# Kernel tuning notes

Measured on AMD Instinct MI355X. Metric: run time of the kernel, lower is better.

## Reference

```python
import jax, jax.numpy as jnp
import numpy as np

# ---- module hyperparameters (match init_kwargs) ----
SPATIAL = (32, 64)          # token grid, N = 32*64 = 2048
D_MODEL = 1024
N_HEADS = 16
HEAD_DIM = D_MODEL // N_HEADS  # 64
THETA = 10000.0
XPOS_SCALE_BASE = SPATIAL[0] * 2  # 64


def _rope_tables():
    """ND rotary (xpos) tables, lucidrains-style.
    Each spatial axis gets head_dim//ndim rotary channels; frequencies are
    interleave-repeated (r=2) to pair with rotate_half. Returns cos, sin,
    xpos scale, each [N, HEAD_DIM] float32."""
    nd = len(SPATIAL)
    dpa = HEAD_DIM // nd  # dims per axis (32)
    freqs_axes, scale_axes = [], []
    for size in SPATIAL:
        inv_freq = 1.0 / (THETA ** (np.arange(0, dpa, 2, dtype=np.float64) / dpa))
        t = np.arange(size, dtype=np.float64)
        f = np.repeat(t[:, None] * inv_freq[None, :], 2, axis=-1)        # [size, dpa]
        sbase = (np.arange(0, dpa, 2, dtype=np.float64) + 0.4 * dpa) / (1.4 * dpa)
        power = (t - size // 2) / XPOS_SCALE_BASE
        sc = np.repeat(sbase[None, :] ** power[:, None], 2, axis=-1)     # [size, dpa]
        freqs_axes.append(f)
        scale_axes.append(sc)
    # broadcast each axis table over the full grid, concat along channel dim
    def grid_concat(tabs):
        parts = []
        for i, tab in enumerate(tabs):
            shp = [1] * nd + [dpa]
            shp[i] = SPATIAL[i]
            parts.append(np.broadcast_to(tab.reshape(shp), tuple(SPATIAL) + (dpa,)))
        return np.concatenate(parts, axis=-1).reshape(-1, HEAD_DIM)  # [N, HEAD_DIM]
    freqs = grid_concat(freqs_axes)
    xscale = grid_concat(scale_axes)
    return (jnp.asarray(np.cos(freqs), jnp.float32),
            jnp.asarray(np.sin(freqs), jnp.float32),
            jnp.asarray(xscale, jnp.float32))


def _rotate_half(x):
    # pairwise rotation: (x1, x2) -> (-x2, x1), interleaved layout
    x = x.reshape(*x.shape[:-1], -1, 2)
    x1, x2 = x[..., 0], x[..., 1]
    return jnp.stack((-x2, x1), axis=-1).reshape(*x.shape[:-2], -1)


def setup_inputs() -> dict:
    key = jax.random.key(0)
    ks = jax.random.split(key, 3)
    B, N = 2, SPATIAL[0] * SPATIAL[1]
    x = jax.random.normal(ks[0], (B, N, D_MODEL), dtype=jnp.float32)
    w_qkv = jax.random.normal(ks[1], (D_MODEL, 3 * D_MODEL), dtype=jnp.float32) * 0.02
    b_qkv = jnp.zeros((3 * D_MODEL,), jnp.float32)
    w_proj = jax.random.normal(ks[2], (D_MODEL, D_MODEL), dtype=jnp.float32) * 0.02
    b_proj = jnp.zeros((D_MODEL,), jnp.float32)
    return {"x": x, "w_qkv": w_qkv, "b_qkv": b_qkv, "w_proj": w_proj, "b_proj": b_proj}


def reference(x, w_qkv, b_qkv, w_proj, b_proj):
    B, N, C = x.shape
    scale = HEAD_DIM ** -0.5
    qkv = (x @ w_qkv + b_qkv).reshape(B, N, 3, N_HEADS, HEAD_DIM)
    qkv = qkv.transpose(2, 0, 3, 1, 4)  # [3, B, H, N, D]
    q, k, v = qkv[0], qkv[1], qkv[2]
    cos, sin, xs = _rope_tables()       # [N, D], broadcast over B,H
    q = (q * cos + _rotate_half(q) * sin) * xs
    k = (k * cos + _rotate_half(k) * sin) / xs
    attn = jax.nn.softmax(jnp.einsum('bhnd,bhmd->bhnm', q, k) * scale, axis=-1)
    out = jnp.einsum('bhnm,bhmd->bhnd', attn, v)
    out = out.transpose(0, 2, 1, 3).reshape(B, N, C)
    return out @ w_proj + b_proj
```

## Files before the change

kernel.cpp:

```cpp
#include <hip/hip_runtime.h>
#include <math.h>

typedef __attribute__((ext_vector_type(8))) _Float16 f16x8;
typedef __attribute__((ext_vector_type(4))) _Float16 f16x4;
typedef __attribute__((ext_vector_type(4))) float f32x4;

#define MFMAH(a, b, c) __builtin_amdgcn_mfma_f32_16x16x32_f16((a), (b), (c), 0, 0, 0)

#define QSCALE 0.18033688011112042f
#define SOFF 4.328085122666891f


__global__ void cast_f16_kernel(const float* __restrict__ in, _Float16* __restrict__ out, int n) {
    int i = blockIdx.x * 256 + threadIdx.x;
    if (i >= n) return;
    out[i] = (_Float16)in[i];
}

__global__ void transpose_cast_f16_kernel(const float* __restrict__ in,
                                          _Float16* __restrict__ out, int C) {
    int i = blockIdx.x * 256 + threadIdx.x;
    if (i >= (C << 10)) return;
    int c = i >> 10;
    int r = i & 1023;
    out[i] = (_Float16)in[(size_t)r * C + c];
}

__global__ void rope_tables_kernel(float* __restrict__ ct, float* __restrict__ st,
                                   float* __restrict__ xt) {
    int i = blockIdx.x * 256 + threadIdx.x;
    if (i >= 2048 * 64) return;
    int n = i >> 6, d = i & 63;
    int gi = n >> 6, gj = n & 63;
    int axis = d >> 5;
    int p = (d & 31) >> 1;
    float t = axis ? (float)gj : (float)gi;
    float half = axis ? 32.0f : 16.0f;
    float inv_freq = powf(10000.0f, -(float)p * (1.0f / 16.0f));
    float fr = t * inv_freq;
    float sbase = (2.0f * p + 12.8f) / 44.8f;
    float xs = powf(sbase, (t - half) * (1.0f / 64.0f));
    ct[i] = cosf(fr);
    st[i] = sinf(fr);
    xt[i] = xs;
}

#define LDK 40

__global__ __launch_bounds__(256) void gemm_qkv_kernel(
    const _Float16* __restrict__ A_g, const _Float16* __restrict__ B_g,
    const float* __restrict__ bias, const float* __restrict__ ctab,
    const float* __restrict__ stab, const float* __restrict__ xtab,
    _Float16* __restrict__ qb, _Float16* __restrict__ kb, _Float16* __restrict__ vt) {
    __shared__ __align__(16) _Float16 Asm[128 * LDK];
    __shared__ __align__(16) _Float16 Bsm[128 * LDK];

    const int tid = threadIdx.x;
    const int lane = tid & 63, wave = tid >> 6;
    const int quad = lane >> 4, l16 = lane & 15;
    const int wm = wave >> 1, wn = wave & 1;
    const int m0 = blockIdx.x * 128, n0 = blockIdx.y * 128;

    f32x4 zero = {0.f, 0.f, 0.f, 0.f};
    f32x4 acc[4][4];
#pragma unroll
    for (int i = 0; i < 4; ++i)
#pragma unroll
        for (int j = 0; j < 4; ++j) acc[i][j] = zero;

    const int r0 = tid >> 2, o0 = (tid & 3) << 3;
    const int r1 = (tid + 256) >> 2, o1 = ((tid + 256) & 3) << 3;

    for (int k0 = 0; k0 < 1024; k0 += 32) {
        const size_t ab = (size_t)m0 * 1024 + k0;
        const size_t bb = (size_t)n0 * 1024 + k0;
        *(f16x8*)&Asm[r0 * LDK + o0] = *(const f16x8*)&A_g[ab + (size_t)r0 * 1024 + o0];
        *(f16x8*)&Asm[r1 * LDK + o1] = *(const f16x8*)&A_g[ab + (size_t)r1 * 1024 + o1];
        *(f16x8*)&Bsm[r0 * LDK + o0] = *(const f16x8*)&B_g[bb + (size_t)r0 * 1024 + o0];
        *(f16x8*)&Bsm[r1 * LDK + o1] = *(const f16x8*)&B_g[bb + (size_t)r1 * 1024 + o1];
        __syncthreads();

        f16x8 af[4], bf[4];
#pragma unroll
        for (int i = 0; i < 4; ++i) {
            af[i] = *(const f16x8*)&Asm[(wm * 64 + i * 16 + l16) * LDK + quad * 8];
            bf[i] = *(const f16x8*)&Bsm[(wn * 64 + i * 16 + l16) * LDK + quad * 8];
        }
#pragma unroll
        for (int i = 0; i < 4; ++i)
#pragma unroll
            for (int j = 0; j < 4; ++j) acc[i][j] = MFMAH(af[i], bf[j], acc[i][j]);
        __syncthreads();
    }

    float bj[4];
#pragma unroll
    for (int j = 0; j < 4; ++j) bj[j] = bias[n0 + wn * 64 + j * 16 + l16];

    if (n0 < 2048) {
#pragma unroll
        for (int i = 0; i < 4; ++i) {
#pragma unroll
            for (int r = 0; r < 4; ++r) {
                const int row = m0 + wm * 64 + i * 16 + quad * 4 + r;
                const int b = row >> 11, nrow = row & 2047;
#pragma unroll
                for (int j = 0; j < 4; ++j) {
                    const int col = n0 + wn * 64 + j * 16 + l16;
                    float v = acc[i][j][r] + bj[j];
                    float partner = __shfl_xor(v, 1);
                    const int hh = (col >> 6) & 15;
                    const int d = col & 63;
                    const size_t o = ((size_t)(b * 16 + hh) * 2048 + nrow) * 64 + d;
                    float rh = (d & 1) ? partner : -partner;
                    const int ti = nrow * 64 + d;
                    float rv = v * ctab[ti] + rh * stab[ti];
                    float xs = xtab[ti];
                    if (col < 1024)
                        qb[o] = (_Float16)(rv * xs * QSCALE);
                    else
                        kb[o] = (_Float16)(rv / xs);
                }
            }
        }
    } else {
#pragma unroll
        for (int i = 0; i < 4; ++i) {
            const int row = m0 + wm * 64 + i * 16 + quad * 4;
            const int b = row >> 11, nrow = row & 2047;
#pragma unroll
            for (int j = 0; j < 4; ++j) {
                const int col = n0 + wn * 64 + j * 16 + l16;
                const int hh = (col >> 6) & 15;
                const int d = col & 63;
                f16x4 pv4;
#pragma unroll
                for (int r = 0; r < 4; ++r) pv4[r] = (_Float16)(acc[i][j][r] + bj[j]);
                *(f16x4*)&vt[((size_t)(b * 16 + hh) * 64 + d) * 2048 + nrow] = pv4;
            }
        }
    }
}

__global__ __launch_bounds__(256) void gemm_proj_kernel(
    const _Float16* __restrict__ A_g, const _Float16* __restrict__ B_g,
    const float* __restrict__ bias, float* __restrict__ out) {
    __shared__ __align__(16) _Float16 Asm[128 * LDK];
    __shared__ __align__(16) _Float16 Bsm[128 * LDK];

    const int tid = threadIdx.x;
    const int lane = tid & 63, wave = tid >> 6;
    const int quad = lane >> 4, l16 = lane & 15;
    const int wm = wave >> 1, wn = wave & 1;
    const int m0 = blockIdx.x * 128, n0 = blockIdx.y * 128;

    f32x4 zero = {0.f, 0.f, 0.f, 0.f};
    f32x4 acc[4][4];
#pragma unroll
    for (int i = 0; i < 4; ++i)
#pragma unroll
        for (int j = 0; j < 4; ++j) acc[i][j] = zero;

    const int r0 = tid >> 2, o0 = (tid & 3) << 3;
    const int r1 = (tid + 256) >> 2, o1 = ((tid + 256) & 3) << 3;

    for (int k0 = 0; k0 < 1024; k0 += 32) {
        const size_t ab = (size_t)m0 * 1024 + k0;
        const size_t bb = (size_t)n0 * 1024 + k0;
        *(f16x8*)&Asm[r0 * LDK + o0] = *(const f16x8*)&A_g[ab + (size_t)r0 * 1024 + o0];
        *(f16x8*)&Asm[r1 * LDK + o1] = *(const f16x8*)&A_g[ab + (size_t)r1 * 1024 + o1];
        *(f16x8*)&Bsm[r0 * LDK + o0] = *(const f16x8*)&B_g[bb + (size_t)r0 * 1024 + o0];
        *(f16x8*)&Bsm[r1 * LDK + o1] = *(const f16x8*)&B_g[bb + (size_t)r1 * 1024 + o1];
        __syncthreads();

        f16x8 af[4], bf[4];
#pragma unroll
        for (int i = 0; i < 4; ++i) {
            af[i] = *(const f16x8*)&Asm[(wm * 64 + i * 16 + l16) * LDK + quad * 8];
            bf[i] = *(const f16x8*)&Bsm[(wn * 64 + i * 16 + l16) * LDK + quad * 8];
        }
#pragma unroll
        for (int i = 0; i < 4; ++i)
#pragma unroll
            for (int j = 0; j < 4; ++j) acc[i][j] = MFMAH(af[i], bf[j], acc[i][j]);
        __syncthreads();
    }

    float bj[4];
#pragma unroll
    for (int j = 0; j < 4; ++j) bj[j] = bias[n0 + wn * 64 + j * 16 + l16];
#pragma unroll
    for (int i = 0; i < 4; ++i)
#pragma unroll
        for (int r = 0; r < 4; ++r) {
            const int row = m0 + wm * 64 + i * 16 + quad * 4 + r;
#pragma unroll
            for (int j = 0; j < 4; ++j) {
                const int col = n0 + wn * 64 + j * 16 + l16;
                out[(size_t)row * 1024 + col] = acc[i][j][r] + bj[j];
            }
        }
}

#define KLD 72
#define PLD 72

__global__ __launch_bounds__(256) void attn_kernel(
    const _Float16* __restrict__ qb, const _Float16* __restrict__ kb,
    const _Float16* __restrict__ vt, _Float16* __restrict__ ao) {
    __shared__ __align__(16) _Float16 Ksm[64 * KLD];
    __shared__ __align__(16) _Float16 Vsm[64 * KLD];
    __shared__ __align__(16) _Float16 Psm[4 * 32 * PLD];

    const int tid = threadIdx.x;
    const int lane = tid & 63, wave = tid >> 6;
    const int quad = lane >> 4, l16 = lane & 15;
    const int qt = blockIdx.x & 15, bh = blockIdx.x >> 4;
    const size_t base = (size_t)bh * 2048 * 64;
    const int qrow0 = qt * 128 + wave * 32;

    f16x8 qf[2][2];
#pragma unroll
    for (int rg = 0; rg < 2; ++rg) {
        qf[rg][0] = *(const f16x8*)&qb[base + (size_t)(qrow0 + rg * 16 + l16) * 64 + quad * 8];
        qf[rg][1] = *(const f16x8*)&qb[base + (size_t)(qrow0 + rg * 16 + l16) * 64 + 32 + quad * 8];
    }

    f32x4 zero = {0.f, 0.f, 0.f, 0.f};
    f32x4 moff = {-SOFF, -SOFF, -SOFF, -SOFF};
    f32x4 o[2][4];
    float lsum[2] = {0.f, 0.f};
#pragma unroll
    for (int rg = 0; rg < 2; ++rg)
#pragma unroll
        for (int dc = 0; dc < 4; ++dc) o[rg][dc] = zero;

    const int kr0 = tid >> 3, ko0 = (tid & 7) << 3;
    const int kr1 = (tid + 256) >> 3, ko1 = ((tid + 256) & 7) << 3;
    f16x8 pk[2], pv[2];

    pk[0] = *(const f16x8*)&kb[base + (size_t)kr0 * 64 + ko0];
    pk[1] = *(const f16x8*)&kb[base + (size_t)kr1 * 64 + ko1];
    pv[0] = *(const f16x8*)&vt[((size_t)bh * 64 + kr0) * 2048 + ko0];
    pv[1] = *(const f16x8*)&vt[((size_t)bh * 64 + kr1) * 2048 + ko1];

    _Float16* Pw = &Psm[wave * 32 * PLD];

    for (int it = 0; it < 32; ++it) {
        __syncthreads();
        *(f16x8*)&Ksm[kr0 * KLD + ko0] = pk[0];
        *(f16x8*)&Ksm[kr1 * KLD + ko1] = pk[1];
        *(f16x8*)&Vsm[kr0 * KLD + ko0] = pv[0];
        *(f16x8*)&Vsm[kr1 * KLD + ko1] = pv[1];
        __syncthreads();

        if (it + 1 < 32) {
            const int kt = (it + 1) * 64;
            pk[0] = *(const f16x8*)&kb[base + (size_t)(kt + kr0) * 64 + ko0];
            pk[1] = *(const f16x8*)&kb[base + (size_t)(kt + kr1) * 64 + ko1];
            pv[0] = *(const f16x8*)&vt[((size_t)bh * 64 + kr0) * 2048 + kt + ko0];
            pv[1] = *(const f16x8*)&vt[((size_t)bh * 64 + kr1) * 2048 + kt + ko1];
        }

        f32x4 s[2][4];
#pragma unroll
        for (int kg = 0; kg < 4; ++kg) {
            f16x8 kf0 = *(const f16x8*)&Ksm[(kg * 16 + l16) * KLD + quad * 8];
            f16x8 kf1 = *(const f16x8*)&Ksm[(kg * 16 + l16) * KLD + 32 + quad * 8];
            s[0][kg] = MFMAH(kf0, qf[0][0], moff);
            s[0][kg] = MFMAH(kf1, qf[0][1], s[0][kg]);
            s[1][kg] = MFMAH(kf0, qf[1][0], moff);
            s[1][kg] = MFMAH(kf1, qf[1][1], s[1][kg]);
        }

#pragma unroll
        for (int rg = 0; rg < 2; ++rg)
#pragma unroll
            for (int kg = 0; kg < 4; ++kg) {
                float p0 = __builtin_amdgcn_exp2f(s[rg][kg][0]);
                float p1 = __builtin_amdgcn_exp2f(s[rg][kg][1]);
                float p2 = __builtin_amdgcn_exp2f(s[rg][kg][2]);
                float p3 = __builtin_amdgcn_exp2f(s[rg][kg][3]);
                lsum[rg] += (p0 + p1) + (p2 + p3);
                f16x4 ph = {(_Float16)p0, (_Float16)p1, (_Float16)p2, (_Float16)p3};
                *(f16x4*)&Pw[(rg * 16 + l16) * PLD + kg * 16 + quad * 4] = ph;
            }

        f16x8 pf[2][2];
#pragma unroll
        for (int rg = 0; rg < 2; ++rg) {
            pf[rg][0] = *(const f16x8*)&Pw[(rg * 16 + l16) * PLD + quad * 8];
            pf[rg][1] = *(const f16x8*)&Pw[(rg * 16 + l16) * PLD + 32 + quad * 8];
        }
#pragma unroll
        for (int dc = 0; dc < 4; ++dc) {
            f16x8 vf0 = *(const f16x8*)&Vsm[(dc * 16 + l16) * KLD + quad * 8];
            f16x8 vf1 = *(const f16x8*)&Vsm[(dc * 16 + l16) * KLD + 32 + quad * 8];
#pragma unroll
            for (int rg = 0; rg < 2; ++rg) {
                o[rg][dc] = MFMAH(pf[rg][0], vf0, o[rg][dc]);
                o[rg][dc] = MFMAH(pf[rg][1], vf1, o[rg][dc]);
            }
        }
    }

    float linv[2][4];
#pragma unroll
    for (int rg = 0; rg < 2; ++rg) {
        float v = lsum[rg];
        v += __shfl_xor(v, 16);
        v += __shfl_xor(v, 32);
        v = 1.0f / v;
#pragma unroll
        for (int r = 0; r < 4; ++r) linv[rg][r] = __shfl(v, quad * 4 + r);
    }

    const int b = bh >> 4, hh = bh & 15;
#pragma unroll
    for (int rg = 0; rg < 2; ++rg)
#pragma unroll
        for (int dc = 0; dc < 4; ++dc)
#pragma unroll
            for (int r = 0; r < 4; ++r) {
                float v = o[rg][dc][r] * linv[rg][r];
                const int qrow = qrow0 + rg * 16 + quad * 4 + r;
                const size_t oi = ((size_t)(b * 2048 + qrow)) * 1024 + hh * 64 + dc * 16 + l16;
                ao[oi] = (_Float16)v;
            }
}

extern "C" void kernel_launch(void* const* d_in, const int* in_sizes, int n_in,
                              void* d_out, int out_size, void* d_ws, size_t ws_size,
                              hipStream_t stream) {
    const float* x = (const float*)d_in[0];
    const float* w_qkv = (const float*)d_in[1];
    const float* b_qkv = (const float*)d_in[2];
    const float* w_proj = (const float*)d_in[3];
    const float* b_proj = (const float*)d_in[4];
    float* out = (float*)d_out;

    char* ws = (char*)d_ws;
    size_t off = 0;
    auto take = [&](size_t bytes) { char* p = ws + off; off += bytes; return p; };
    _Float16* xbuf   = (_Float16*)take(8388608);
    _Float16* wqkvT  = (_Float16*)take(6291456);
    _Float16* wprojT = (_Float16*)take(2097152);
    _Float16* qbuf   = (_Float16*)take(8388608);
    _Float16* kbuf   = (_Float16*)take(8388608);
    _Float16* vtbuf  = (_Float16*)take(8388608);
    float* ctab      = (float*)take(524288);
    float* stab      = (float*)take(524288);
    float* xtab      = (float*)take(524288);
    _Float16* ao = xbuf;

    cast_f16_kernel<<<16384, 256, 0, stream>>>(x, xbuf, 4194304);
    transpose_cast_f16_kernel<<<12288, 256, 0, stream>>>(w_qkv, wqkvT, 3072);
    transpose_cast_f16_kernel<<<4096, 256, 0, stream>>>(w_proj, wprojT, 1024);
    rope_tables_kernel<<<512, 256, 0, stream>>>(ctab, stab, xtab);
    gemm_qkv_kernel<<<dim3(32, 24), 256, 0, stream>>>(xbuf, wqkvT, b_qkv,
                                                      ctab, stab, xtab, qbuf, kbuf, vtbuf);
    attn_kernel<<<512, 256, 0, stream>>>(qbuf, kbuf, vtbuf, ao);
    gemm_proj_kernel<<<dim3(32, 8), 256, 0, stream>>>(ao, wprojT, b_proj, out);
}
```

Measured before the change: 241.5 us.

## Double-buffer LDS in GEMMs and attention, fuse prep kernels, retile projection

Merges the four preprocessing kernels (casts, weight transposes, RoPE tables) into one launch. The QKV GEMM, projection GEMM and attention kernel now double-buffer shared memory, so the global loads for the next tile overlap MFMA work on the current one. The projection GEMM drops to 128x64 tiles to launch more blocks, and the attention block index is reordered so consecutive blocks cover different heads. This costs more LDS per block, which may lower occupancy.

After: 217.3 us. 1.11x faster.

```diff
diff --git a/kernel.cpp b/kernel.cpp
--- a/kernel.cpp
+++ b/kernel.cpp
@@ -10,39 +10,39 @@
 #define QSCALE 0.18033688011112042f
 #define SOFF 4.328085122666891f
 
-
-__global__ void cast_f16_kernel(const float* __restrict__ in, _Float16* __restrict__ out, int n) {
-    int i = blockIdx.x * 256 + threadIdx.x;
-    if (i >= n) return;
-    out[i] = (_Float16)in[i];
-}
-
-__global__ void transpose_cast_f16_kernel(const float* __restrict__ in,
-                                          _Float16* __restrict__ out, int C) {
-    int i = blockIdx.x * 256 + threadIdx.x;
-    if (i >= (C << 10)) return;
-    int c = i >> 10;
-    int r = i & 1023;
-    out[i] = (_Float16)in[(size_t)r * C + c];
-}
-
-__global__ void rope_tables_kernel(float* __restrict__ ct, float* __restrict__ st,
-                                   float* __restrict__ xt) {
-    int i = blockIdx.x * 256 + threadIdx.x;
-    if (i >= 2048 * 64) return;
-    int n = i >> 6, d = i & 63;
-    int gi = n >> 6, gj = n & 63;
-    int axis = d >> 5;
-    int p = (d & 31) >> 1;
-    float t = axis ? (float)gj : (float)gi;
-    float half = axis ? 32.0f : 16.0f;
-    float inv_freq = powf(10000.0f, -(float)p * (1.0f / 16.0f));
-    float fr = t * inv_freq;
-    float sbase = (2.0f * p + 12.8f) / 44.8f;
-    float xs = powf(sbase, (t - half) * (1.0f / 64.0f));
-    ct[i] = cosf(fr);
-    st[i] = sinf(fr);
-    xt[i] = xs;
+__global__ void prep_kernel(const float* __restrict__ x, const float* __restrict__ w_qkv,
+                            const float* __restrict__ w_proj, _Float16* __restrict__ xb,
+                            _Float16* __restrict__ wq, _Float16* __restrict__ wp,
+                            float* __restrict__ ct, float* __restrict__ st,
+                            float* __restrict__ xt) {
+    const int b = blockIdx.x, tid = threadIdx.x;
+    if (b < 16384) {
+        int i = b * 256 + tid;
+        xb[i] = (_Float16)x[i];
+    } else if (b < 28672) {
+        int i = (b - 16384) * 256 + tid;
+        int c = i >> 10, r = i & 1023;
+        wq[i] = (_Float16)w_qkv[(size_t)r * 3072 + c];
+    } else if (b < 32768) {
+        int i = (b - 28672) * 256 + tid;
+        int c = i >> 10, r = i & 1023;
+        wp[i] = (_Float16)w_proj[(size_t)r * 1024 + c];
+    } else {
+        int i = (b - 32768) * 256 + tid;
+        int n = i >> 6, d = i & 63;
+        int gi = n >> 6, gj = n & 63;
+        int axis = d >> 5;
+        int p = (d & 31) >> 1;
+        float t = axis ? (float)gj : (float)gi;
+        float half = axis ? 32.0f : 16.0f;
+        float inv_freq = powf(10000.0f, -(float)p * (1.0f / 16.0f));
+        float fr = t * inv_freq;
+        float sbase = (2.0f * p + 12.8f) / 44.8f;
+        float xs = powf(sbase, (t - half) * (1.0f / 64.0f));
+        ct[i] = cosf(fr);
+        st[i] = sinf(fr);
+        xt[i] = xs;
+    }
 }
 
 #define LDK 40
@@ -52,8 +52,8 @@
     const float* __restrict__ bias, const float* __restrict__ ctab,
     const float* __restrict__ stab, const float* __restrict__ xtab,
     _Float16* __restrict__ qb, _Float16* __restrict__ kb, _Float16* __restrict__ vt) {
-    __shared__ __align__(16) _Float16 Asm[128 * LDK];
-    __shared__ __align__(16) _Float16 Bsm[128 * LDK];
+    __shared__ __align__(16) _Float16 Asm0[128 * LDK], Asm1[128 * LDK];
+    __shared__ __align__(16) _Float16 Bsm0[128 * LDK], Bsm1[128 * LDK];
 
     const int tid = threadIdx.x;
     const int lane = tid & 63, wave = tid >> 6;
@@ -69,27 +69,48 @@
         for (int j = 0; j < 4; ++j) acc[i][j] = zero;
 
     const int r0 = tid >> 2, o0 = (tid & 3) << 3;
-    const int r1 = (tid + 256) >> 2, o1 = ((tid + 256) & 3) << 3;
-
-    for (int k0 = 0; k0 < 1024; k0 += 32) {
-        const size_t ab = (size_t)m0 * 1024 + k0;
-        const size_t bb = (size_t)n0 * 1024 + k0;
-        *(f16x8*)&Asm[r0 * LDK + o0] = *(const f16x8*)&A_g[ab + (size_t)r0 * 1024 + o0];
-        *(f16x8*)&Asm[r1 * LDK + o1] = *(const f16x8*)&A_g[ab + (size_t)r1 * 1024 + o1];
-        *(f16x8*)&Bsm[r0 * LDK + o0] = *(const f16x8*)&B_g[bb + (size_t)r0 * 1024 + o0];
-        *(f16x8*)&Bsm[r1 * LDK + o1] = *(const f16x8*)&B_g[bb + (size_t)r1 * 1024 + o1];
-        __syncthreads();
-
+    const size_t ab = (size_t)m0 * 1024;
+    const size_t bb = (size_t)n0 * 1024;
+
+    f16x8 pa0, pa1, pb0, pb1;
+    auto gload = [&](int k) {
+        pa0 = *(const f16x8*)&A_g[ab + k + (size_t)r0 * 1024 + o0];
+        pa1 = *(const f16x8*)&A_g[ab + k + (size_t)(r0 + 64) * 1024 + o0];
+        pb0 = *(const f16x8*)&B_g[bb + k + (size_t)r0 * 1024 + o0];
+        pb1 = *(const f16x8*)&B_g[bb + k + (size_t)(r0 + 64) * 1024 + o0];
+    };
+    auto stage = [&](_Float16* As, _Float16* Bs) {
+        *(f16x8*)&As[r0 * LDK + o0] = pa0;
+        *(f16x8*)&As[(r0 + 64) * LDK + o0] = pa1;
+        *(f16x8*)&Bs[r0 * LDK + o0] = pb0;
+        *(f16x8*)&Bs[(r0 + 64) * LDK + o0] = pb1;
+    };
+    auto compute = [&](const _Float16* As, const _Float16* Bs) {
         f16x8 af[4], bf[4];
 #pragma unroll
         for (int i = 0; i < 4; ++i) {
-            af[i] = *(const f16x8*)&Asm[(wm * 64 + i * 16 + l16) * LDK + quad * 8];
-            bf[i] = *(const f16x8*)&Bsm[(wn * 64 + i * 16 + l16) * LDK + quad * 8];
+            af[i] = *(const f16x8*)&As[(wm * 64 + i * 16 + l16) * LDK + quad * 8];
+            bf[i] = *(const f16x8*)&Bs[(wn * 64 + i * 16 + l16) * LDK + quad * 8];
         }
 #pragma unroll
         for (int i = 0; i < 4; ++i)
 #pragma unroll
             for (int j = 0; j < 4; ++j) acc[i][j] = MFMAH(af[i], bf[j], acc[i][j]);
+    };
+
+    gload(0);
+    stage(Asm0, Bsm0);
+    gload(32);
+    __syncthreads();
+
+    for (int it = 0; it < 32; it += 2) {
+        stage(Asm1, Bsm1);
+        if (it + 2 < 32) gload((it + 2) * 32);
+        compute(Asm0, Bsm0);
+        __syncthreads();
+        if (it + 2 < 32) stage(Asm0, Bsm0);
+        if (it + 3 < 32) gload((it + 3) * 32);
+        compute(Asm1, Bsm1);
         __syncthreads();
     }
 
@@ -145,58 +166,78 @@
 __global__ __launch_bounds__(256) void gemm_proj_kernel(
     const _Float16* __restrict__ A_g, const _Float16* __restrict__ B_g,
     const float* __restrict__ bias, float* __restrict__ out) {
-    __shared__ __align__(16) _Float16 Asm[128 * LDK];
-    __shared__ __align__(16) _Float16 Bsm[128 * LDK];
+    __shared__ __align__(16) _Float16 Asm0[128 * LDK], Asm1[128 * LDK];
+    __shared__ __align__(16) _Float16 Bsm0[64 * LDK], Bsm1[64 * LDK];
 
     const int tid = threadIdx.x;
     const int lane = tid & 63, wave = tid >> 6;
     const int quad = lane >> 4, l16 = lane & 15;
     const int wm = wave >> 1, wn = wave & 1;
-    const int m0 = blockIdx.x * 128, n0 = blockIdx.y * 128;
+    const int m0 = blockIdx.x * 128, n0 = blockIdx.y * 64;
 
     f32x4 zero = {0.f, 0.f, 0.f, 0.f};
-    f32x4 acc[4][4];
+    f32x4 acc[4][2];
 #pragma unroll
     for (int i = 0; i < 4; ++i)
 #pragma unroll
-        for (int j = 0; j < 4; ++j) acc[i][j] = zero;
+        for (int j = 0; j < 2; ++j) acc[i][j] = zero;
 
     const int r0 = tid >> 2, o0 = (tid & 3) << 3;
-    const int r1 = (tid + 256) >> 2, o1 = ((tid + 256) & 3) << 3;
-
-    for (int k0 = 0; k0 < 1024; k0 += 32) {
-        const size_t ab = (size_t)m0 * 1024 + k0;
-        const size_t bb = (size_t)n0 * 1024 + k0;
-        *(f16x8*)&Asm[r0 * LDK + o0] = *(const f16x8*)&A_g[ab + (size_t)r0 * 1024 + o0];
-        *(f16x8*)&Asm[r1 * LDK + o1] = *(const f16x8*)&A_g[ab + (size_t)r1 * 1024 + o1];
-        *(f16x8*)&Bsm[r0 * LDK + o0] = *(const f16x8*)&B_g[bb + (size_t)r0 * 1024 + o0];
-        *(f16x8*)&Bsm[r1 * LDK + o1] = *(const f16x8*)&B_g[bb + (size_t)r1 * 1024 + o1];
-        __syncthreads();
-
-        f16x8 af[4], bf[4];
-#pragma unroll
-        for (int i = 0; i < 4; ++i) {
-            af[i] = *(const f16x8*)&Asm[(wm * 64 + i * 16 + l16) * LDK + quad * 8];
-            bf[i] = *(const f16x8*)&Bsm[(wn * 64 + i * 16 + l16) * LDK + quad * 8];
-        }
+    const size_t ab = (size_t)m0 * 1024;
+    const size_t bb = (size_t)n0 * 1024;
+
+    f16x8 pa0, pa1, pb0;
+    auto gload = [&](int k) {
+        pa0 = *(const f16x8*)&A_g[ab + k + (size_t)r0 * 1024 + o0];
+        pa1 = *(const f16x8*)&A_g[ab + k + (size_t)(r0 + 64) * 1024 + o0];
+        pb0 = *(const f16x8*)&B_g[bb + k + (size_t)r0 * 1024 + o0];
+    };
+    auto stage = [&](_Float16* As, _Float16* Bs) {
+        *(f16x8*)&As[r0 * LDK + o0] = pa0;
+        *(f16x8*)&As[(r0 + 64) * LDK + o0] = pa1;
+        if (r0 < 64) *(f16x8*)&Bs[r0 * LDK + o0] = pb0;
+    };
+    auto compute = [&](const _Float16* As, const _Float16* Bs) {
+        f16x8 af[4], bf[2];
 #pragma unroll
         for (int i = 0; i < 4; ++i)
-#pragma unroll
-            for (int j = 0; j < 4; ++j) acc[i][j] = MFMAH(af[i], bf[j], acc[i][j]);
-        __syncthreads();
-    }
-
-    float bj[4];
-#pragma unroll
-    for (int j = 0; j < 4; ++j) bj[j] = bias[n0 + wn * 64 + j * 16 + l16];
+            af[i] = *(const f16x8*)&As[(wm * 64 + i * 16 + l16) * LDK + quad * 8];
+#pragma unroll
+        for (int j = 0; j < 2; ++j)
+            bf[j] = *(const f16x8*)&Bs[(wn * 32 + j * 16 + l16) * LDK + quad * 8];
+#pragma unroll
+        for (int i = 0; i < 4; ++i)
+#pragma unroll
+            for (int j = 0; j < 2; ++j) acc[i][j] = MFMAH(af[i], bf[j], acc[i][j]);
+    };
+
+    gload(0);
+    stage(Asm0, Bsm0);
+    gload(32);
+    __syncthreads();
+
+    for (int it = 0; it < 32; it += 2) {
+        stage(Asm1, Bsm1);
+        if (it + 2 < 32) gload((it + 2) * 32);
+        compute(Asm0, Bsm0);
+        __syncthreads();
+        if (it + 2 < 32) stage(Asm0, Bsm0);
+        if (it + 3 < 32) gload((it + 3) * 32);
+        compute(Asm1, Bsm1);
+        __syncthreads();
+    }
+
+    float bj[2];
+#pragma unroll
+    for (int j = 0; j < 2; ++j) bj[j] = bias[n0 + wn * 32 + j * 16 + l16];
 #pragma unroll
     for (int i = 0; i < 4; ++i)
 #pragma unroll
         for (int r = 0; r < 4; ++r) {
             const int row = m0 + wm * 64 + i * 16 + quad * 4 + r;
 #pragma unroll
-            for (int j = 0; j < 4; ++j) {
-                const int col = n0 + wn * 64 + j * 16 + l16;
+            for (int j = 0; j < 2; ++j) {
+                const int col = n0 + wn * 32 + j * 16 + l16;
                 out[(size_t)row * 1024 + col] = acc[i][j][r] + bj[j];
             }
         }
@@ -208,14 +249,14 @@
 __global__ __launch_bounds__(256) void attn_kernel(
     const _Float16* __restrict__ qb, const _Float16* __restrict__ kb,
     const _Float16* __restrict__ vt, _Float16* __restrict__ ao) {
-    __shared__ __align__(16) _Float16 Ksm[64 * KLD];
-    __shared__ __align__(16) _Float16 Vsm[64 * KLD];
+    __shared__ __align__(16) _Float16 Ksm0[64 * KLD], Ksm1[64 * KLD];
+    __shared__ __align__(16) _Float16 Vsm0[64 * KLD], Vsm1[64 * KLD];
     __shared__ __align__(16) _Float16 Psm[4 * 32 * PLD];
 
     const int tid = threadIdx.x;
     const int lane = tid & 63, wave = tid >> 6;
     const int quad = lane >> 4, l16 = lane & 15;
-    const int qt = blockIdx.x & 15, bh = blockIdx.x >> 4;
+    const int bh = blockIdx.x & 31, qt = blockIdx.x >> 5;
     const size_t base = (size_t)bh * 2048 * 64;
     const int qrow0 = qt * 128 + wave * 32;
 
@@ -226,8 +267,8 @@
         qf[rg][1] = *(const f16x8*)&qb[base + (size_t)(qrow0 + rg * 16 + l16) * 64 + 32 + quad * 8];
     }
 
+    f32x4 moff = {-SOFF, -SOFF, -SOFF, -SOFF};
     f32x4 zero = {0.f, 0.f, 0.f, 0.f};
-    f32x4 moff = {-SOFF, -SOFF, -SOFF, -SOFF};
     f32x4 o[2][4];
     float lsum[2] = {0.f, 0.f};
 #pragma unroll
@@ -236,43 +277,34 @@
         for (int dc = 0; dc < 4; ++dc) o[rg][dc] = zero;
 
     const int kr0 = tid >> 3, ko0 = (tid & 7) << 3;
-    const int kr1 = (tid + 256) >> 3, ko1 = ((tid + 256) & 7) << 3;
-    f16x8 pk[2], pv[2];
-
-    pk[0] = *(const f16x8*)&kb[base + (size_t)kr0 * 64 + ko0];
-    pk[1] = *(const f16x8*)&kb[base + (size_t)kr1 * 64 + ko1];
-    pv[0] = *(const f16x8*)&vt[((size_t)bh * 64 + kr0) * 2048 + ko0];
-    pv[1] = *(const f16x8*)&vt[((size_t)bh * 64 + kr1) * 2048 + ko1];
+    const int kr1 = kr0 + 32;
+    f16x8 pk0, pk1, pv0, pv1;
+    auto gload = [&](int kt) {
+        pk0 = *(const f16x8*)&kb[base + (size_t)(kt + kr0) * 64 + ko0];
+        pk1 = *(const f16x8*)&kb[base + (size_t)(kt + kr1) * 64 + ko0];
+        pv0 = *(const f16x8*)&vt[((size_t)bh * 64 + kr0) * 2048 + kt + ko0];
+        pv1 = *(const f16x8*)&vt[((size_t)bh * 64 + kr1) * 2048 + kt + ko0];
+    };
+    auto stage = [&](_Float16* Ks, _Float16* Vs) {
+        *(f16x8*)&Ks[kr0 * KLD + ko0] = pk0;
+        *(f16x8*)&Ks[kr1 * KLD + ko0] = pk1;
+        *(f16x8*)&Vs[kr0 * KLD + ko0] = pv0;
+        *(f16x8*)&Vs[kr1 * KLD + ko0] = pv1;
+    };
 
     _Float16* Pw = &Psm[wave * 32 * PLD];
 
-    for (int it = 0; it < 32; ++it) {
-        __syncthreads();
-        *(f16x8*)&Ksm[kr0 * KLD + ko0] = pk[0];
-        *(f16x8*)&Ksm[kr1 * KLD + ko1] = pk[1];
-        *(f16x8*)&Vsm[kr0 * KLD + ko0] = pv[0];
-        *(f16x8*)&Vsm[kr1 * KLD + ko1] = pv[1];
-        __syncthreads();
-
-        if (it + 1 < 32) {
-            const int kt = (it + 1) * 64;
-            pk[0] = *(const f16x8*)&kb[base + (size_t)(kt + kr0) * 64 + ko0];
-            pk[1] = *(const f16x8*)&kb[base + (size_t)(kt + kr1) * 64 + ko1];
-            pv[0] = *(const f16x8*)&vt[((size_t)bh * 64 + kr0) * 2048 + kt + ko0];
-            pv[1] = *(const f16x8*)&vt[((size_t)bh * 64 + kr1) * 2048 + kt + ko1];
-        }
-
+    auto compute = [&](const _Float16* Ks, const _Float16* Vs) {
         f32x4 s[2][4];
 #pragma unroll
         for (int kg = 0; kg < 4; ++kg) {
-            f16x8 kf0 = *(const f16x8*)&Ksm[(kg * 16 + l16) * KLD + quad * 8];
-            f16x8 kf1 = *(const f16x8*)&Ksm[(kg * 16 + l16) * KLD + 32 + quad * 8];
+            f16x8 kf0 = *(const f16x8*)&Ks[(kg * 16 + l16) * KLD + quad * 8];
+            f16x8 kf1 = *(const f16x8*)&Ks[(kg * 16 + l16) * KLD + 32 + quad * 8];
             s[0][kg] = MFMAH(kf0, qf[0][0], moff);
             s[0][kg] = MFMAH(kf1, qf[0][1], s[0][kg]);
             s[1][kg] = MFMAH(kf0, qf[1][0], moff);
             s[1][kg] = MFMAH(kf1, qf[1][1], s[1][kg]);
         }
-
 #pragma unroll
         for (int rg = 0; rg < 2; ++rg)
 #pragma unroll
@@ -285,7 +317,6 @@
                 f16x4 ph = {(_Float16)p0, (_Float16)p1, (_Float16)p2, (_Float16)p3};
                 *(f16x4*)&Pw[(rg * 16 + l16) * PLD + kg * 16 + quad * 4] = ph;
             }
-
         f16x8 pf[2][2];
 #pragma unroll
         for (int rg = 0; rg < 2; ++rg) {
@@ -294,14 +325,30 @@
         }
 #pragma unroll
         for (int dc = 0; dc < 4; ++dc) {
-            f16x8 vf0 = *(const f16x8*)&Vsm[(dc * 16 + l16) * KLD + quad * 8];
-            f16x8 vf1 = *(const f16x8*)&Vsm[(dc * 16 + l16) * KLD + 32 + quad * 8];
+            f16x8 vf0 = *(const f16x8*)&Vs[(dc * 16 + l16) * KLD + quad * 8];
+            f16x8 vf1 = *(const f16x8*)&Vs[(dc * 16 + l16) * KLD + 32 + quad * 8];
 #pragma unroll
             for (int rg = 0; rg < 2; ++rg) {
                 o[rg][dc] = MFMAH(pf[rg][0], vf0, o[rg][dc]);
                 o[rg][dc] = MFMAH(pf[rg][1], vf1, o[rg][dc]);
             }
         }
+    };
+
+    gload(0);
+    stage(Ksm0, Vsm0);
+    gload(64);
+    __syncthreads();
+
+    for (int it = 0; it < 32; it += 2) {
+        stage(Ksm1, Vsm1);
+        if (it + 2 < 32) gload((it + 2) * 64);
+        compute(Ksm0, Vsm0);
+        __syncthreads();
+        if (it + 2 < 32) stage(Ksm0, Vsm0);
+        if (it + 3 < 32) gload((it + 3) * 64);
+        compute(Ksm1, Vsm1);
+        __syncthreads();
     }
 
     float linv[2][4];
@@ -353,12 +400,10 @@
     float* xtab      = (float*)take(524288);
     _Float16* ao = xbuf;
 
-    cast_f16_kernel<<<16384, 256, 0, stream>>>(x, xbuf, 4194304);
-    transpose_cast_f16_kernel<<<12288, 256, 0, stream>>>(w_qkv, wqkvT, 3072);
-    transpose_cast_f16_kernel<<<4096, 256, 0, stream>>>(w_proj, wprojT, 1024);
-    rope_tables_kernel<<<512, 256, 0, stream>>>(ctab, stab, xtab);
+    prep_kernel<<<33280, 256, 0, stream>>>(x, w_qkv, w_proj, xbuf, wqkvT, wprojT,
+                                           ctab, stab, xtab);
     gemm_qkv_kernel<<<dim3(32, 24), 256, 0, stream>>>(xbuf, wqkvT, b_qkv,
                                                       ctab, stab, xtab, qbuf, kbuf, vtbuf);
     attn_kernel<<<512, 256, 0, stream>>>(qbuf, kbuf, vtbuf, ao);
-    gemm_proj_kernel<<<dim3(32, 8), 256, 0, stream>>>(ao, wprojT, b_proj, out);
+    gemm_proj_kernel<<<dim3(32, 16), 256, 0, stream>>>(ao, wprojT, b_proj, out);
 }
```
